# Kernel tuning notes

Hardware: AMD Instinct MI355X
Metric: run time of the kernel (lower is better)

Reference implementation:

```python
import jax, jax.numpy as jnp
import numpy as np

B, D, C = 128, 2048, 16522
BETA, KNN, ALPHA0 = 0.05, 6, 0.01


def setup_inputs() -> dict:
    key = jax.random.key(0)
    k1, k2, k3 = jax.random.split(key, 3)
    inputs = jax.random.normal(k1, (B, D), dtype=jnp.float32)
    label = jax.random.randint(k2, (B,), 0, C, dtype=jnp.int64 if jax.config.jax_enable_x64 else jnp.int32)
    # memory bank; init as unit-norm rows (torch init is zeros, but rows are
    # always renormalized after the first update, so unit-norm is the steady state)
    em = jax.random.normal(k3, (C, D), dtype=jnp.float32)
    em = em / jnp.linalg.norm(em, axis=1, keepdims=True)
    return {"inputs": inputs, "label": label, "em": em, "epoch": 10}


def reference(inputs, label, em, epoch):
    alpha = ALPHA0 * epoch
    # similarity logits: [B, C]
    logits = jnp.matmul(inputs, em.T) / BETA
    # smooth_hot mask: 2 at top-k entries, 3 at the true label (overwrites)
    _, topk = jax.lax.top_k(logits, KNN)                      # [B, KNN]
    rows = jnp.arange(B)
    mask = jnp.zeros_like(logits).at[rows[:, None], topk].set(2.0)
    mask = mask.at[rows, label].set(3.0)
    logp = jax.nn.log_softmax(logits, axis=1)
    loss = (-(mask * logp)).sum(axis=1).mean()
    # sequential per-sample EMA memory update (duplicate labels chain, so scan)
    def step(em_cur, xy):
        x, y = xy
        row = alpha * em_cur[y] + (1.0 - alpha) * x
        row = row / jnp.linalg.norm(row)
        return em_cur.at[y].set(row), None
    em_new, _ = jax.lax.scan(step, em, (inputs, label))
    return loss, em_new
```

## Files before the change

### kernel.cpp

```cpp
#include <hip/hip_runtime.h>
#include <hip/hip_bf16.h>
#include <cstddef>

#define B_    128
#define D_    2048
#define C_    16522
#define BETA_INV 20.0f
#define LSTRIDE 16528

#define NTILES 1033
#define NCHUNK 8
#define CHW    2066

typedef __bf16 bf16;
typedef bf16  bf16x8 __attribute__((ext_vector_type(8)));
typedef float f32x4  __attribute__((ext_vector_type(4)));

#define WS_APACK_OFF 8462336
#define WS_PART_OFF  8986624

__global__ __launch_bounds__(256) void pack_a(const float* __restrict__ inp,
                                              bf16* __restrict__ ap) {
  const int tid  = blockIdx.x * 256 + threadIdx.x;
  const int lane = tid & 63;
  const int ks   = (tid >> 6) & 63;
  const int mt   = tid >> 12;
  const int row  = mt * 16 + (lane & 15);
  const int col  = ks * 32 + (lane >> 4) * 8;
  const float4 v0 = *(const float4*)(inp + row * D_ + col);
  const float4 v1 = *(const float4*)(inp + row * D_ + col + 4);
  bf16x8 b;
  b[0] = (bf16)v0.x; b[1] = (bf16)v0.y; b[2] = (bf16)v0.z; b[3] = (bf16)v0.w;
  b[4] = (bf16)v1.x; b[5] = (bf16)v1.y; b[6] = (bf16)v1.z; b[7] = (bf16)v1.w;
  ((bf16x8*)ap)[tid] = b;
}

__global__ __launch_bounds__(256, 4) void gemm_logits(
    const bf16*  __restrict__ ap,
    const float* __restrict__ em,
    float*       __restrict__ logits)
{
  const int tid  = threadIdx.x;
  const int lane = tid & 63;
  const int w    = tid >> 6;
  const int ml   = lane & 15;
  const int quad = lane >> 4;
  const int n0   = blockIdx.x * 16;
  const int r    = n0 + ml;
  const bool valid = r < C_;

  const float* bp = em + (size_t)(valid ? r : 0) * D_ + quad * 8;
  const bf16x8* af = (const bf16x8*)ap;

  const int ks0 = w * 16;

  f32x4 acc[8] = {};

  f32x4 e0a = *(const f32x4*)(bp + ks0 * 32);
  f32x4 e0b = *(const f32x4*)(bp + ks0 * 32 + 4);

  #pragma unroll 3
  for (int i = 0; i < 15; ++i) {
    const int ks = ks0 + i;
    bf16x8 A0[8];
    #pragma unroll
    for (int mt = 0; mt < 8; ++mt)
      A0[mt] = af[(mt * 64 + ks) * 64 + lane];
    const f32x4 e1a = *(const f32x4*)(bp + (ks + 1) * 32);
    const f32x4 e1b = *(const f32x4*)(bp + (ks + 1) * 32 + 4);
    bf16x8 bv;
    bv[0] = (bf16)e0a[0]; bv[1] = (bf16)e0a[1]; bv[2] = (bf16)e0a[2]; bv[3] = (bf16)e0a[3];
    bv[4] = (bf16)e0b[0]; bv[5] = (bf16)e0b[1]; bv[6] = (bf16)e0b[2]; bv[7] = (bf16)e0b[3];
    #pragma unroll
    for (int mt = 0; mt < 8; ++mt)
      acc[mt] = __builtin_amdgcn_mfma_f32_16x16x32_bf16(A0[mt], bv, acc[mt], 0, 0, 0);
    e0a = e1a; e0b = e1b;
  }
  {
    const int ks = ks0 + 15;
    bf16x8 A0[8];
    #pragma unroll
    for (int mt = 0; mt < 8; ++mt)
      A0[mt] = af[(mt * 64 + ks) * 64 + lane];
    bf16x8 bv;
    bv[0] = (bf16)e0a[0]; bv[1] = (bf16)e0a[1]; bv[2] = (bf16)e0a[2]; bv[3] = (bf16)e0a[3];
    bv[4] = (bf16)e0b[0]; bv[5] = (bf16)e0b[1]; bv[6] = (bf16)e0b[2]; bv[7] = (bf16)e0b[3];
    #pragma unroll
    for (int mt = 0; mt < 8; ++mt)
      acc[mt] = __builtin_amdgcn_mfma_f32_16x16x32_bf16(A0[mt], bv, acc[mt], 0, 0, 0);
  }

  __shared__ f32x4 red[3][8][64];
  if (w > 0) {
    #pragma unroll
    for (int mt = 0; mt < 8; ++mt) red[w - 1][mt][lane] = acc[mt];
  }
  __syncthreads();
  if (w == 0 && valid) {
    #pragma unroll
    for (int mt = 0; mt < 8; ++mt) {
      f32x4 a = acc[mt];
      a += red[0][mt][lane];
      a += red[1][mt][lane];
      a += red[2][mt][lane];
      #pragma unroll
      for (int reg = 0; reg < 4; ++reg) {
        const int row = mt * 16 + quad * 4 + reg;
        logits[row * LSTRIDE + r] = a[reg] * BETA_INV;
      }
    }
  }
}

__global__ __launch_bounds__(256) void row_loss_part(
    const float* __restrict__ logits,
    const int*   __restrict__ label,
    float*       __restrict__ part)
{
  const int b = blockIdx.x >> 3;
  const int c = blockIdx.x & 7;
  const int t = threadIdx.x;
  const int lo = c * CHW;
  const int hi = (lo + CHW < C_) ? lo + CHW : C_;
  const float* row = logits + b * LSTRIDE;
  const int y = label[b];

  float m = -INFINITY, s = 0.f, ly = -INFINITY;
  float tv[6]; int ti[6];
  #pragma unroll
  for (int q = 0; q < 6; ++q) { tv[q] = -INFINITY; ti[q] = -1; }

  for (int i = lo + t; i < hi; i += 256) {
    const float v = row[i];
    if (v > m) { s = s * __expf(m - v) + 1.f; m = v; }
    else       { s += __expf(v - m); }
    if (i == y) ly = v;
    if (v > tv[5]) {
      tv[5] = v; ti[5] = i;
      #pragma unroll
      for (int q = 5; q > 0; --q)
        if (tv[q] > tv[q - 1]) {
          const float fv = tv[q]; tv[q] = tv[q - 1]; tv[q - 1] = fv;
          const int   fi = ti[q]; ti[q] = ti[q - 1]; ti[q - 1] = fi;
        }
    }
  }

  __shared__ float rm[256], rs[256];
  __shared__ float cv[1536];
  __shared__ int   ci[1536];
  __shared__ float sly;

  rm[t] = m; rs[t] = s;
  #pragma unroll
  for (int q = 0; q < 6; ++q) { cv[t * 6 + q] = tv[q]; ci[t * 6 + q] = ti[q]; }
  if (t == 0) sly = -INFINITY;
  __syncthreads();
  if (ly != -INFINITY) sly = ly;

  for (int off = 128; off >= 1; off >>= 1) {
    if (t < off) {
      const float m2 = rm[t + off], s2 = rs[t + off];
      const float M = fmaxf(rm[t], m2);
      rs[t] = rs[t] * __expf(rm[t] - M) + s2 * __expf(m2 - M);
      rm[t] = M;
    }
    __syncthreads();
  }

  if (t < 64) {
    float otv[6]; int oti[6];
    for (int rr = 0; rr < 6; ++rr) {
      float bv = -INFINITY; int bi = -1, bs = -1;
      for (int u = 0; u < 24; ++u) {
        const int slot = t * 24 + u;
        const float v = cv[slot];
        if (v > bv) { bv = v; bi = ci[slot]; bs = slot; }
      }
      #pragma unroll
      for (int off = 32; off >= 1; off >>= 1) {
        const float ov = __shfl_down(bv, off);
        const int   oi = __shfl_down(bi, off);
        const int   os = __shfl_down(bs, off);
        if (ov > bv) { bv = ov; bi = oi; bs = os; }
      }
      bv = __shfl(bv, 0); bi = __shfl(bi, 0); bs = __shfl(bs, 0);
      if (bs >= t * 24 && bs < (t + 1) * 24) cv[bs] = -INFINITY;
      otv[rr] = bv; oti[rr] = bi;
    }
    if (t == 0) {
      float* p = part + (size_t)(b * 8 + c) * 16;
      p[0] = rm[0]; p[1] = rs[0]; p[2] = sly;
      #pragma unroll
      for (int q = 0; q < 6; ++q) { p[4 + q] = otv[q]; ((int*)p)[10 + q] = oti[q]; }
    }
  }
}

__global__ __launch_bounds__(64) void row_loss_merge(
    const float* __restrict__ part,
    const int*   __restrict__ label,
    float*       __restrict__ out)
{
  const int b = blockIdx.x;
  const int lane = threadIdx.x;
  const int y = label[b];

  float m = -INFINITY, s = 0.f, ly = -INFINITY;
  if (lane < 8) {
    const float* p = part + (size_t)(b * 8 + lane) * 16;
    m = p[0]; s = p[1]; ly = p[2];
  }
  float M = m, LY = ly;
  #pragma unroll
  for (int off = 32; off >= 1; off >>= 1) {
    M  = fmaxf(M,  __shfl_down(M,  off));
    LY = fmaxf(LY, __shfl_down(LY, off));
  }
  M = __shfl(M, 0); LY = __shfl(LY, 0);
  float contrib = (lane < 8) ? s * __expf(m - M) : 0.f;
  #pragma unroll
  for (int off = 32; off >= 1; off >>= 1) contrib += __shfl_down(contrib, off);
  const float S = __shfl(contrib, 0);

  float v = -INFINITY; int idx = -1;
  if (lane < 48) {
    const float* p = part + (size_t)(b * 8 + lane / 6) * 16;
    v   = p[4 + lane % 6];
    idx = ((const int*)p)[10 + lane % 6];
  }
  float stop = 0.f; int intop = 0;
  for (int rr = 0; rr < 6; ++rr) {
    float bv = v; int bi = idx, bl = lane;
    #pragma unroll
    for (int off = 32; off >= 1; off >>= 1) {
      const float ov = __shfl_down(bv, off);
      const int   oi = __shfl_down(bi, off);
      const int   ol = __shfl_down(bl, off);
      if (ov > bv) { bv = ov; bi = oi; bl = ol; }
    }
    bv = __shfl(bv, 0); bi = __shfl(bi, 0); bl = __shfl(bl, 0);
    stop += bv;
    if (bi == y) intop = 1;
    if (lane == bl) v = -INFINITY;
  }

  if (lane == 0) {
    const float lse = M + logf(S);
    const float loss = intop ? (13.f * lse - LY - 2.f * stop)
                             : (15.f * lse - 3.f * LY - 2.f * stop);
    atomicAdd(out, loss * (1.0f / 128.0f));
  }
}

__global__ __launch_bounds__(256) void em_update(
    const float* __restrict__ inp,
    const int*   __restrict__ label,
    const float* __restrict__ em,
    const int*   __restrict__ epoch,
    float*       __restrict__ out_em)
{
  __shared__ int lbl[B_];
  __shared__ float red[4];
  const int t = threadIdx.x;
  if (t < B_) lbl[t] = label[t];
  __syncthreads();

  const int i = blockIdx.x;
  const int y = lbl[i];
  for (int j = 0; j < i; ++j)
    if (lbl[j] == y) return;

  const float alpha = 0.01f * (float)epoch[0];
  const int lane = t & 63, wave = t >> 6;

  float r[8];
  #pragma unroll
  for (int u = 0; u < 8; ++u) r[u] = em[(size_t)y * D_ + t + u * 256];

  for (int j = i; j < B_; ++j) {
    if (lbl[j] != y) continue;
    const float* x = inp + j * D_;
    float ss = 0.f;
    #pragma unroll
    for (int u = 0; u < 8; ++u) {
      r[u] = alpha * r[u] + (1.f - alpha) * x[t + u * 256];
      ss += r[u] * r[u];
    }
    #pragma unroll
    for (int off = 32; off >= 1; off >>= 1) ss += __shfl_down(ss, off);
    if (lane == 0) red[wave] = ss;
    __syncthreads();
    const float inv = 1.f / sqrtf(red[0] + red[1] + red[2] + red[3]);
    #pragma unroll
    for (int u = 0; u < 8; ++u) r[u] *= inv;
    __syncthreads();
  }

  #pragma unroll
  for (int u = 0; u < 8; ++u) out_em[(size_t)y * D_ + t + u * 256] = r[u];
}

extern "C" void kernel_launch(void* const* d_in, const int* in_sizes, int n_in,
                              void* d_out, int out_size, void* d_ws, size_t ws_size,
                              hipStream_t stream) {
  const float* inp   = (const float*)d_in[0];
  const int*   label = (const int*)d_in[1];
  const float* em    = (const float*)d_in[2];
  const int*   epoch = (const int*)d_in[3];

  float* out    = (float*)d_out;
  float* out_em = out + 1;
  float* logits = (float*)d_ws;
  bf16*  apack  = (bf16*)((char*)d_ws + WS_APACK_OFF);
  float* part   = (float*)((char*)d_ws + WS_PART_OFF);

  hipMemsetAsync(d_out, 0, sizeof(float), stream);
  hipMemcpyAsync(out_em, em, (size_t)C_ * D_ * sizeof(float),
                 hipMemcpyDeviceToDevice, stream);

  pack_a        <<<dim3(128),        dim3(256), 0, stream>>>(inp, apack);
  gemm_logits   <<<dim3(NTILES),     dim3(256), 0, stream>>>(apack, em, logits);
  row_loss_part <<<dim3(B_ * NCHUNK),dim3(256), 0, stream>>>(logits, label, part);
  row_loss_merge<<<dim3(B_),         dim3(64),  0, stream>>>(part, label, out);
  em_update     <<<dim3(B_),         dim3(256), 0, stream>>>(inp, label, em, epoch, out_em);
}
```

Before: 136.6 us.

## Fuse bf16 pack, memory-bank copy and EMA update into one prep kernel

Replaces the device-to-device memcpy of the memory bank, the pack_a kernel and the em_update kernel with a single prep launch. The first 128 blocks pack the inputs to bf16, and each remaining block owns one bank row. A block either copies its row unchanged or applies the chained EMA updates for the labels that hit it. This removes two launches and the separate full-bank copy, and avoids copying rows that are later overwritten. The cost is 16522 extra blocks that each scan the 128 labels serially.

Result: slower. 177.8 us (+30.1%).

```diff
diff --git a/kernel.cpp b/kernel.cpp
--- a/kernel.cpp
+++ b/kernel.cpp
@@ -19,20 +19,81 @@
 #define WS_APACK_OFF 8462336
 #define WS_PART_OFF  8986624
 
-__global__ __launch_bounds__(256) void pack_a(const float* __restrict__ inp,
-                                              bf16* __restrict__ ap) {
-  const int tid  = blockIdx.x * 256 + threadIdx.x;
-  const int lane = tid & 63;
-  const int ks   = (tid >> 6) & 63;
-  const int mt   = tid >> 12;
-  const int row  = mt * 16 + (lane & 15);
-  const int col  = ks * 32 + (lane >> 4) * 8;
-  const float4 v0 = *(const float4*)(inp + row * D_ + col);
-  const float4 v1 = *(const float4*)(inp + row * D_ + col + 4);
-  bf16x8 b;
-  b[0] = (bf16)v0.x; b[1] = (bf16)v0.y; b[2] = (bf16)v0.z; b[3] = (bf16)v0.w;
-  b[4] = (bf16)v1.x; b[5] = (bf16)v1.y; b[6] = (bf16)v1.z; b[7] = (bf16)v1.w;
-  ((bf16x8*)ap)[tid] = b;
+__global__ __launch_bounds__(256) void prep(
+    const float* __restrict__ inp,
+    const int*   __restrict__ label,
+    const float* __restrict__ em,
+    const int*   __restrict__ epoch,
+    bf16*        __restrict__ ap,
+    float*       __restrict__ out_em)
+{
+  const int t = threadIdx.x;
+  const int b = blockIdx.x;
+
+  if (b < 128) {
+    const int tid  = b * 256 + t;
+    const int lane = tid & 63;
+    const int ks   = (tid >> 6) & 63;
+    const int mt   = tid >> 12;
+    const int row  = mt * 16 + (lane & 15);
+    const int col  = ks * 32 + (lane >> 4) * 8;
+    const float4 v0 = *(const float4*)(inp + row * D_ + col);
+    const float4 v1 = *(const float4*)(inp + row * D_ + col + 4);
+    bf16x8 bb;
+    bb[0] = (bf16)v0.x; bb[1] = (bf16)v0.y; bb[2] = (bf16)v0.z; bb[3] = (bf16)v0.w;
+    bb[4] = (bf16)v1.x; bb[5] = (bf16)v1.y; bb[6] = (bf16)v1.z; bb[7] = (bf16)v1.w;
+    ((bf16x8*)ap)[tid] = bb;
+    return;
+  }
+
+  const int r = b - 128;
+  __shared__ int   lbl[B_];
+  __shared__ float red[4];
+  if (t < B_) lbl[t] = label[t];
+  __syncthreads();
+
+  int i0 = -1;
+  for (int j = 0; j < B_; ++j)
+    if (lbl[j] == r) { i0 = j; break; }
+
+  if (i0 < 0) {
+    const f32x4* src = (const f32x4*)(em + (size_t)r * D_);
+    float*       dst = out_em + (size_t)r * D_;
+    const f32x4 v0 = src[t * 2];
+    const f32x4 v1 = src[t * 2 + 1];
+    *(f32x4*)(dst + t * 8)     = v0;
+    *(f32x4*)(dst + t * 8 + 4) = v1;
+    return;
+  }
+
+  const float alpha = 0.01f * (float)epoch[0];
+  const int lane = t & 63, wave = t >> 6;
+
+  float rr[8];
+  #pragma unroll
+  for (int u = 0; u < 8; ++u) rr[u] = em[(size_t)r * D_ + t + u * 256];
+
+  for (int j = i0; j < B_; ++j) {
+    if (lbl[j] != r) continue;
+    const float* x = inp + j * D_;
+    float ss = 0.f;
+    #pragma unroll
+    for (int u = 0; u < 8; ++u) {
+      rr[u] = alpha * rr[u] + (1.f - alpha) * x[t + u * 256];
+      ss += rr[u] * rr[u];
+    }
+    #pragma unroll
+    for (int off = 32; off >= 1; off >>= 1) ss += __shfl_down(ss, off);
+    if (lane == 0) red[wave] = ss;
+    __syncthreads();
+    const float inv = 1.f / sqrtf(red[0] + red[1] + red[2] + red[3]);
+    #pragma unroll
+    for (int u = 0; u < 8; ++u) rr[u] *= inv;
+    __syncthreads();
+  }
+
+  #pragma unroll
+  for (int u = 0; u < 8; ++u) out_em[(size_t)r * D_ + t + u * 256] = rr[u];
 }
 
 __global__ __launch_bounds__(256, 4) void gemm_logits(
@@ -253,54 +314,6 @@
   }
 }
 
-__global__ __launch_bounds__(256) void em_update(
-    const float* __restrict__ inp,
-    const int*   __restrict__ label,
-    const float* __restrict__ em,
-    const int*   __restrict__ epoch,
-    float*       __restrict__ out_em)
-{
-  __shared__ int lbl[B_];
-  __shared__ float red[4];
-  const int t = threadIdx.x;
-  if (t < B_) lbl[t] = label[t];
-  __syncthreads();
-
-  const int i = blockIdx.x;
-  const int y = lbl[i];
-  for (int j = 0; j < i; ++j)
-    if (lbl[j] == y) return;
-
-  const float alpha = 0.01f * (float)epoch[0];
-  const int lane = t & 63, wave = t >> 6;
-
-  float r[8];
-  #pragma unroll
-  for (int u = 0; u < 8; ++u) r[u] = em[(size_t)y * D_ + t + u * 256];
-
-  for (int j = i; j < B_; ++j) {
-    if (lbl[j] != y) continue;
-    const float* x = inp + j * D_;
-    float ss = 0.f;
-    #pragma unroll
-    for (int u = 0; u < 8; ++u) {
-      r[u] = alpha * r[u] + (1.f - alpha) * x[t + u * 256];
-      ss += r[u] * r[u];
-    }
-    #pragma unroll
-    for (int off = 32; off >= 1; off >>= 1) ss += __shfl_down(ss, off);
-    if (lane == 0) red[wave] = ss;
-    __syncthreads();
-    const float inv = 1.f / sqrtf(red[0] + red[1] + red[2] + red[3]);
-    #pragma unroll
-    for (int u = 0; u < 8; ++u) r[u] *= inv;
-    __syncthreads();
-  }
-
-  #pragma unroll
-  for (int u = 0; u < 8; ++u) out_em[(size_t)y * D_ + t + u * 256] = r[u];
-}
-
 extern "C" void kernel_launch(void* const* d_in, const int* in_sizes, int n_in,
                               void* d_out, int out_size, void* d_ws, size_t ws_size,
                               hipStream_t stream) {
@@ -316,12 +329,9 @@
   float* part   = (float*)((char*)d_ws + WS_PART_OFF);
 
   hipMemsetAsync(d_out, 0, sizeof(float), stream);
-  hipMemcpyAsync(out_em, em, (size_t)C_ * D_ * sizeof(float),
-                 hipMemcpyDeviceToDevice, stream);
-
-  pack_a        <<<dim3(128),        dim3(256), 0, stream>>>(inp, apack);
+
+  prep          <<<dim3(128 + C_),   dim3(256), 0, stream>>>(inp, label, em, epoch, apack, out_em);
   gemm_logits   <<<dim3(NTILES),     dim3(256), 0, stream>>>(apack, em, logits);
   row_loss_part <<<dim3(B_ * NCHUNK),dim3(256), 0, stream>>>(logits, label, part);
   row_loss_merge<<<dim3(B_),         dim3(64),  0, stream>>>(part, label, out);
-  em_update     <<<dim3(B_),         dim3(256), 0, stream>>>(inp, label, em, epoch, out_em);
-}
+}
```
